# Optimization experiments

Hardware: AMD Instinct MI355X
Metric: run time of the kernel (lower is better)

The kernel has to match this reference:

```python
import jax, jax.numpy as jnp
import numpy as np

N, DIM, T = 131072, 1024, 256  # tokens, signature dim, num_tiles


def setup_inputs() -> dict:
    key = jax.random.key(0)
    k1, k2, k3 = jax.random.split(key, 3)
    x = jax.random.normal(k1, (N, DIM), dtype=jnp.float32)
    base = jax.random.uniform(k2, (DIM,), dtype=jnp.float32, minval=-1.0, maxval=1.0)
    deltas = jax.random.uniform(k3, (T - 1, DIM), dtype=jnp.float32, minval=-0.5, maxval=0.5)
    return {"x": x, "base": base, "deltas": deltas}


def _all_signatures(base, deltas):
    # base signature = sign(base); tile i>0: sig = sign(base*(1-|d|) + d*|d|), d = sign(delta_i)
    b = jnp.sign(base)                       # [DIM]
    d = jnp.sign(deltas)                     # [T-1, DIM]
    ad = jnp.abs(d)                          # |d| in {0,1}
    rest = jnp.sign(b[None, :] * (1.0 - ad) + d * ad)  # [T-1, DIM]
    return jnp.concatenate([b[None, :], rest], axis=0)  # [T, DIM]


def _hamming_distances(x, sigs):
    # 2-bit encoding: bit0 = (v>0), bit1 = (v<0).
    # Hamming dist over bits = sum(a) + sum(b) - 2*dot(a,b) per bit-plane (a^b = a+b-2ab for bits).
    px = (x > 0).astype(jnp.float32)          # [N, DIM]
    nx = (x < 0).astype(jnp.float32)
    ps = (sigs > 0).astype(jnp.float32)       # [T, DIM]
    ns = (sigs < 0).astype(jnp.float32)
    cross = px @ ps.T + nx @ ns.T             # [N, T] (single fused GEMM pair, K=DIM)
    pop_x = (px + nx).sum(axis=-1, keepdims=True)   # [N, 1]
    pop_s = (ps + ns).sum(axis=-1)[None, :]         # [1, T]
    return pop_x + pop_s - 2.0 * cross        # [N, T]


def reference(x, base, deltas):
    sigs = _all_signatures(base, deltas)       # [T, DIM] ternary
    distances = _hamming_distances(x, sigs)    # [N, T] (integer-valued float32)
    tile_idx = jnp.argmin(distances, axis=-1)  # [N]
    return tile_idx, distances
```

## Files before the change

kernel.cpp:

```cpp
#include <hip/hip_runtime.h>

typedef unsigned int u32;

#define NTOK 131072
#define DIMS 1024
#define NT   256

using bf16x8 = __attribute__((ext_vector_type(8))) short;
using f32x4  = __attribute__((ext_vector_type(4))) float;

#define BF_OFF   0
#define SV_OFF   (1 << 20)
#define FLAG_OFF ((1 << 20) + 1024)

__device__ __forceinline__ short sgnbf(float v) {
    return v > 0.f ? (short)0x3F80 : (v < 0.f ? (short)0xBF80 : (short)0);
}
__device__ __forceinline__ short absbf(float v) {
    return v != 0.f ? (short)0x3F80 : (short)0;
}

__global__ void sig_kernel(const float* __restrict__ base,
                           const float* __restrict__ deltas,
                           short* __restrict__ Bf,
                           float* __restrict__ Sv,
                           int* __restrict__ flags)
{
    const int t  = blockIdx.x;
    const int l  = threadIdx.x;
    const int ks = l >> 1;
    int nz = 0, zany = 0;
    #pragma unroll
    for (int gh = 0; gh < 2; ++gh) {
        const int g = (l & 1) * 2 + gh;
        bf16x8 a8, u8;
        #pragma unroll
        for (int j = 0; j < 8; ++j) {
            const int d  = ks * 32 + g * 8 + j;
            const float b  = base[d];
            const float dl = (t > 0) ? deltas[(size_t)(t - 1) * DIMS + d] : 0.f;
            const float s  = (dl != 0.f) ? dl : b;
            a8[j] = sgnbf(s);
            u8[j] = absbf(s);
            nz   += (s != 0.f) ? 1 : 0;
            zany |= (s == 0.f) ? 1 : 0;
        }
        const int L    = g * 16 + (t & 15);
        const int n    = t >> 4;
        const int slot = n ^ (t & 15);
        const size_t off = (size_t)L * 128 + slot * 8;
        *(bf16x8*)(Bf + (((size_t)0 * 32 + ks) << 13) + off) = a8;
        *(bf16x8*)(Bf + (((size_t)1 * 32 + ks) << 13) + off) = u8;
    }
    #pragma unroll
    for (int off = 1; off < 64; off <<= 1) nz += __shfl_xor(nz, off);
    const bool za = __any(zany != 0);
    if (l == 0) { Sv[t] = (float)nz; flags[t] = za ? 1 : 0; }
}

__global__ __launch_bounds__(256, 2)
void dist_kernel(const float* __restrict__ x,
                 const short* __restrict__ Bf,
                 const float* __restrict__ Sv,
                 const int* __restrict__ flags,
                 float* __restrict__ idx_out,
                 float* __restrict__ dist_out)
{
    __shared__ short lds[2][16384];

    const int lane = threadIdx.x & 63;
    const int w    = threadIdx.x >> 6;
    const int tok0 = blockIdx.x * 128 + w * 32;
    const int mrow = lane & 15;
    const int g    = lane >> 4;

    const int ff = flags[lane] | flags[64 + lane] | flags[128 + lane] | flags[192 + lane];
    const bool sigz = __any(ff != 0);

    const float* __restrict__ xr0 = x + (size_t)(tok0 + mrow) * DIMS + g * 8;
    const float* __restrict__ xr1 = x + (size_t)(tok0 + 16 + mrow) * DIMS + g * 8;

    f32x4 acc0[16], acc1[16];
    #pragma unroll
    for (int n = 0; n < 16; ++n) {
        acc0[n] = (f32x4){0.f, 0.f, 0.f, 0.f};
        acc1[n] = (f32x4){0.f, 0.f, 0.f, 0.f};
    }

    auto STAGE = [&](int b, int p, int kb) {
        #pragma unroll
        for (int s = 0; s < 2; ++s) {
            const short* src = Bf + (((size_t)p * 32 + 2 * kb + s) << 13) + w * 2048 + lane * 8;
            #pragma unroll
            for (int i = 0; i < 4; ++i) {
                __builtin_amdgcn_global_load_lds(
                    (const __attribute__((address_space(1))) u32*)(src + i * 512),
                    (__attribute__((address_space(3))) u32*)(&lds[b][s * 8192 + w * 2048 + i * 512]),
                    16, 0, 0);
            }
        }
    };

    int nz0 = 0, nz1 = 0;
    const int nplanes = sigz ? 2 : 1;

    for (int p = 0; p < nplanes; ++p) {
        STAGE(0, p, 0);
        float4 xv[8];
        xv[0] = *(const float4*)(xr0);       xv[1] = *(const float4*)(xr0 + 4);
        xv[2] = *(const float4*)(xr0 + 32);  xv[3] = *(const float4*)(xr0 + 36);
        xv[4] = *(const float4*)(xr1);       xv[5] = *(const float4*)(xr1 + 4);
        xv[6] = *(const float4*)(xr1 + 32);  xv[7] = *(const float4*)(xr1 + 36);

        for (int kb = 0; kb < 16; ++kb) {
            __syncthreads();

            float4 nx[8];
            if (kb < 15) {
                STAGE((kb + 1) & 1, p, kb + 1);
                const int o = (kb + 1) * 64;
                nx[0] = *(const float4*)(xr0 + o);      nx[1] = *(const float4*)(xr0 + o + 4);
                nx[2] = *(const float4*)(xr0 + o + 32); nx[3] = *(const float4*)(xr0 + o + 36);
                nx[4] = *(const float4*)(xr1 + o);      nx[5] = *(const float4*)(xr1 + o + 4);
                nx[6] = *(const float4*)(xr1 + o + 32); nx[7] = *(const float4*)(xr1 + o + 36);
            }

            if (p == 1) {
                #pragma unroll
                for (int i = 0; i < 4; ++i) {
                    nz0 += (xv[i][0]!=0.f)+(xv[i][1]!=0.f)+(xv[i][2]!=0.f)+(xv[i][3]!=0.f);
                    nz1 += (xv[4+i][0]!=0.f)+(xv[4+i][1]!=0.f)+(xv[4+i][2]!=0.f)+(xv[4+i][3]!=0.f);
                }
            }

            #pragma unroll
            for (int s = 0; s < 2; ++s) {
                const float4 a0 = xv[2 * s], a1 = xv[2 * s + 1];
                const float4 b0 = xv[4 + 2 * s], b1 = xv[4 + 2 * s + 1];
                bf16x8 f0, f1;
                if (p == 0) {
                    f0[0]=sgnbf(a0.x); f0[1]=sgnbf(a0.y); f0[2]=sgnbf(a0.z); f0[3]=sgnbf(a0.w);
                    f0[4]=sgnbf(a1.x); f0[5]=sgnbf(a1.y); f0[6]=sgnbf(a1.z); f0[7]=sgnbf(a1.w);
                    f1[0]=sgnbf(b0.x); f1[1]=sgnbf(b0.y); f1[2]=sgnbf(b0.z); f1[3]=sgnbf(b0.w);
                    f1[4]=sgnbf(b1.x); f1[5]=sgnbf(b1.y); f1[6]=sgnbf(b1.z); f1[7]=sgnbf(b1.w);
                } else {
                    f0[0]=absbf(a0.x); f0[1]=absbf(a0.y); f0[2]=absbf(a0.z); f0[3]=absbf(a0.w);
                    f0[4]=absbf(a1.x); f0[5]=absbf(a1.y); f0[6]=absbf(a1.z); f0[7]=absbf(a1.w);
                    f1[0]=absbf(b0.x); f1[1]=absbf(b0.y); f1[2]=absbf(b0.z); f1[3]=absbf(b0.w);
                    f1[4]=absbf(b1.x); f1[5]=absbf(b1.y); f1[6]=absbf(b1.z); f1[7]=absbf(b1.w);
                }

                const short* sa = &lds[kb & 1][s * 8192];
                __builtin_amdgcn_s_setprio(1);
                #pragma unroll
                for (int n = 0; n < 16; ++n) {
                    const bf16x8 ba = *(const bf16x8*)(sa + lane * 128 + ((n ^ mrow) & 15) * 8);
                    acc0[n] = __builtin_amdgcn_mfma_f32_16x16x32_bf16(f0, ba, acc0[n], 0, 0, 0);
                    acc1[n] = __builtin_amdgcn_mfma_f32_16x16x32_bf16(f1, ba, acc1[n], 0, 0, 0);
                }
                __builtin_amdgcn_s_setprio(0);
            }

            #pragma unroll
            for (int i = 0; i < 8; ++i) xv[i] = nx[i];
        }
        __syncthreads();
    }

    float su0r[4], su1r[4];
    if (sigz) {
        nz0 += __shfl_xor(nz0, 16); nz0 += __shfl_xor(nz0, 32);
        nz1 += __shfl_xor(nz1, 16); nz1 += __shfl_xor(nz1, 32);
        const float s0 = (float)nz0, s1 = (float)nz1;
        #pragma unroll
        for (int r = 0; r < 4; ++r) {
            su0r[r] = __shfl(s0, g * 4 + r);
            su1r[r] = __shfl(s1, g * 4 + r);
        }
    }

    int key0[4] = {0x7fffffff,0x7fffffff,0x7fffffff,0x7fffffff};
    int key1[4] = {0x7fffffff,0x7fffffff,0x7fffffff,0x7fffffff};
    #pragma unroll
    for (int n = 0; n < 16; ++n) {
        const int tile = n * 16 + mrow;
        const float svv = sigz ? Sv[tile] : 0.f;
        #pragma unroll
        for (int r = 0; r < 4; ++r) {
            const float dv0 = sigz ? (su0r[r] + svv - acc0[n][r]) : (1024.f - acc0[n][r]);
            const float dv1 = sigz ? (su1r[r] + svv - acc1[n][r]) : (1024.f - acc1[n][r]);
            dist_out[(size_t)(tok0 + g * 4 + r) * NT + tile]      = dv0;
            dist_out[(size_t)(tok0 + 16 + g * 4 + r) * NT + tile] = dv1;
            key0[r] = min(key0[r], ((int)dv0 << 8) | tile);
            key1[r] = min(key1[r], ((int)dv1 << 8) | tile);
        }
    }
    #pragma unroll
    for (int off = 1; off < 16; off <<= 1) {
        #pragma unroll
        for (int r = 0; r < 4; ++r) {
            key0[r] = min(key0[r], __shfl_xor(key0[r], off));
            key1[r] = min(key1[r], __shfl_xor(key1[r], off));
        }
    }
    if (mrow == 0) {
        #pragma unroll
        for (int r = 0; r < 4; ++r) {
            idx_out[tok0 + g * 4 + r]      = (float)(key0[r] & 255);
            idx_out[tok0 + 16 + g * 4 + r] = (float)(key1[r] & 255);
        }
    }
}

extern "C" void kernel_launch(void* const* d_in, const int* in_sizes, int n_in,
                              void* d_out, int out_size, void* d_ws, size_t ws_size,
                              hipStream_t stream)
{
    const float* x      = (const float*)d_in[0];
    const float* base   = (const float*)d_in[1];
    const float* deltas = (const float*)d_in[2];

    short* Bf  = (short*)((char*)d_ws + BF_OFF);
    float* Sv  = (float*)((char*)d_ws + SV_OFF);
    int* flags = (int*)((char*)d_ws + FLAG_OFF);

    float* idx_out  = (float*)d_out;
    float* dist_out = idx_out + NTOK;

    sig_kernel<<<NT, 64, 0, stream>>>(base, deltas, Bf, Sv, flags);
    dist_kernel<<<NTOK / 128, 256, 0, stream>>>(x, Bf, Sv, flags, idx_out, dist_out);
}
```

Measured before the change: 189.1 us.

## Deepen x prefetch to two stages with explicit vmcnt waits in the no-zero path

For the common case where signatures have no zeros, the main loop now keeps three register buffers of x, loading two k-blocks ahead. It replaces __syncthreads with an explicit partial s_waitcnt vmcnt plus s_barrier, and uses sched_barrier to pin the order of LDS staging, conversion and MFMA issue. The goal is to hide global-load latency for x and the LDS fill behind the MFMA work. The cost is more live registers, and the hand-counted vmcnt value is fragile if the compiler changes how many loads it emits. The zero-containing path keeps the old two-plane loop but drops setprio.

```diff
diff --git a/kernel.cpp b/kernel.cpp
--- a/kernel.cpp
+++ b/kernel.cpp
@@ -101,70 +101,123 @@
         }
     };
 
+    auto XLOAD = [&](float4* dst, int kb) {
+        const int o = kb * 64;
+        dst[0] = *(const float4*)(xr0 + o);      dst[1] = *(const float4*)(xr0 + o + 4);
+        dst[2] = *(const float4*)(xr0 + o + 32); dst[3] = *(const float4*)(xr0 + o + 36);
+        dst[4] = *(const float4*)(xr1 + o);      dst[5] = *(const float4*)(xr1 + o + 4);
+        dst[6] = *(const float4*)(xr1 + o + 32); dst[7] = *(const float4*)(xr1 + o + 36);
+    };
+
     int nz0 = 0, nz1 = 0;
-    const int nplanes = sigz ? 2 : 1;
-
-    for (int p = 0; p < nplanes; ++p) {
-        STAGE(0, p, 0);
-        float4 xv[8];
-        xv[0] = *(const float4*)(xr0);       xv[1] = *(const float4*)(xr0 + 4);
-        xv[2] = *(const float4*)(xr0 + 32);  xv[3] = *(const float4*)(xr0 + 36);
-        xv[4] = *(const float4*)(xr1);       xv[5] = *(const float4*)(xr1 + 4);
-        xv[6] = *(const float4*)(xr1 + 32);  xv[7] = *(const float4*)(xr1 + 36);
+
+    if (!sigz) {
+        float4 xv0[8], xv1[8], xv2[8];
+        #pragma unroll
+        for (int i = 0; i < 8; ++i) xv2[i] = (float4){0.f, 0.f, 0.f, 0.f};
+
+        STAGE(0, 0, 0);
+        __builtin_amdgcn_sched_barrier(0);
+        XLOAD(xv0, 0);
+        __builtin_amdgcn_sched_barrier(0);
+        XLOAD(xv1, 1);
+        __builtin_amdgcn_sched_barrier(0);
 
         for (int kb = 0; kb < 16; ++kb) {
+            if (kb < 15) asm volatile("s_waitcnt vmcnt(8)" ::: "memory");
+            else         asm volatile("s_waitcnt vmcnt(0)" ::: "memory");
+            __builtin_amdgcn_s_barrier();
+            __builtin_amdgcn_sched_barrier(0);
+
+            if (kb < 15) STAGE((kb + 1) & 1, 0, kb + 1);
+            __builtin_amdgcn_sched_barrier(0);
+
+            bf16x8 fA0, fA1, fB0, fB1;
+            #pragma unroll
+            for (int j = 0; j < 4; ++j) {
+                fA0[j]     = sgnbf(xv0[0][j]); fA0[4 + j] = sgnbf(xv0[1][j]);
+                fB0[j]     = sgnbf(xv0[2][j]); fB0[4 + j] = sgnbf(xv0[3][j]);
+                fA1[j]     = sgnbf(xv0[4][j]); fA1[4 + j] = sgnbf(xv0[5][j]);
+                fB1[j]     = sgnbf(xv0[6][j]); fB1[4 + j] = sgnbf(xv0[7][j]);
+            }
+
+            if (kb < 14) XLOAD(xv2, kb + 2);
+            __builtin_amdgcn_sched_barrier(0);
+
+            const short* sa0 = &lds[kb & 1][0];
+            const short* sa1 = &lds[kb & 1][8192];
+            __builtin_amdgcn_s_setprio(1);
+            #pragma unroll
+            for (int n = 0; n < 16; ++n) {
+                const bf16x8 ba = *(const bf16x8*)(sa0 + lane * 128 + ((n ^ mrow) & 15) * 8);
+                acc0[n] = __builtin_amdgcn_mfma_f32_16x16x32_bf16(fA0, ba, acc0[n], 0, 0, 0);
+                acc1[n] = __builtin_amdgcn_mfma_f32_16x16x32_bf16(fA1, ba, acc1[n], 0, 0, 0);
+            }
+            #pragma unroll
+            for (int n = 0; n < 16; ++n) {
+                const bf16x8 ba = *(const bf16x8*)(sa1 + lane * 128 + ((n ^ mrow) & 15) * 8);
+                acc0[n] = __builtin_amdgcn_mfma_f32_16x16x32_bf16(fB0, ba, acc0[n], 0, 0, 0);
+                acc1[n] = __builtin_amdgcn_mfma_f32_16x16x32_bf16(fB1, ba, acc1[n], 0, 0, 0);
+            }
+            __builtin_amdgcn_s_setprio(0);
+
+            #pragma unroll
+            for (int i = 0; i < 8; ++i) { xv0[i] = xv1[i]; xv1[i] = xv2[i]; }
+        }
+    } else {
+        for (int p = 0; p < 2; ++p) {
+            STAGE(0, p, 0);
+            float4 xv[8];
+            XLOAD(xv, 0);
+
+            for (int kb = 0; kb < 16; ++kb) {
+                __syncthreads();
+
+                float4 nx[8];
+                if (kb < 15) {
+                    STAGE((kb + 1) & 1, p, kb + 1);
+                    XLOAD(nx, kb + 1);
+                }
+
+                if (p == 1) {
+                    #pragma unroll
+                    for (int i = 0; i < 4; ++i) {
+                        nz0 += (xv[i][0]!=0.f)+(xv[i][1]!=0.f)+(xv[i][2]!=0.f)+(xv[i][3]!=0.f);
+                        nz1 += (xv[4+i][0]!=0.f)+(xv[4+i][1]!=0.f)+(xv[4+i][2]!=0.f)+(xv[4+i][3]!=0.f);
+                    }
+                }
+
+                #pragma unroll
+                for (int s = 0; s < 2; ++s) {
+                    const float4 a0 = xv[2 * s], a1 = xv[2 * s + 1];
+                    const float4 b0 = xv[4 + 2 * s], b1 = xv[4 + 2 * s + 1];
+                    bf16x8 f0, f1;
+                    if (p == 0) {
+                        f0[0]=sgnbf(a0.x); f0[1]=sgnbf(a0.y); f0[2]=sgnbf(a0.z); f0[3]=sgnbf(a0.w);
+                        f0[4]=sgnbf(a1.x); f0[5]=sgnbf(a1.y); f0[6]=sgnbf(a1.z); f0[7]=sgnbf(a1.w);
+                        f1[0]=sgnbf(b0.x); f1[1]=sgnbf(b0.y); f1[2]=sgnbf(b0.z); f1[3]=sgnbf(b0.w);
+                        f1[4]=sgnbf(b1.x); f1[5]=sgnbf(b1.y); f1[6]=sgnbf(b1.z); f1[7]=sgnbf(b1.w);
+                    } else {
+                        f0[0]=absbf(a0.x); f0[1]=absbf(a0.y); f0[2]=absbf(a0.z); f0[3]=absbf(a0.w);
+                        f0[4]=absbf(a1.x); f0[5]=absbf(a1.y); f0[6]=absbf(a1.z); f0[7]=absbf(a1.w);
+                        f1[0]=absbf(b0.x); f1[1]=absbf(b0.y); f1[2]=absbf(b0.z); f1[3]=absbf(b0.w);
+                        f1[4]=absbf(b1.x); f1[5]=absbf(b1.y); f1[6]=absbf(b1.z); f1[7]=absbf(b1.w);
+                    }
+
+                    const short* sa = &lds[kb & 1][s * 8192];
+                    #pragma unroll
+                    for (int n = 0; n < 16; ++n) {
+                        const bf16x8 ba = *(const bf16x8*)(sa + lane * 128 + ((n ^ mrow) & 15) * 8);
+                        acc0[n] = __builtin_amdgcn_mfma_f32_16x16x32_bf16(f0, ba, acc0[n], 0, 0, 0);
+                        acc1[n] = __builtin_amdgcn_mfma_f32_16x16x32_bf16(f1, ba, acc1[n], 0, 0, 0);
+                    }
+                }
+
+                #pragma unroll
+                for (int i = 0; i < 8; ++i) xv[i] = nx[i];
+            }
             __syncthreads();
-
-            float4 nx[8];
-            if (kb < 15) {
-                STAGE((kb + 1) & 1, p, kb + 1);
-                const int o = (kb + 1) * 64;
-                nx[0] = *(const float4*)(xr0 + o);      nx[1] = *(const float4*)(xr0 + o + 4);
-                nx[2] = *(const float4*)(xr0 + o + 32); nx[3] = *(const float4*)(xr0 + o + 36);
-                nx[4] = *(const float4*)(xr1 + o);      nx[5] = *(const float4*)(xr1 + o + 4);
-                nx[6] = *(const float4*)(xr1 + o + 32); nx[7] = *(const float4*)(xr1 + o + 36);
-            }
-
-            if (p == 1) {
-                #pragma unroll
-                for (int i = 0; i < 4; ++i) {
-                    nz0 += (xv[i][0]!=0.f)+(xv[i][1]!=0.f)+(xv[i][2]!=0.f)+(xv[i][3]!=0.f);
-                    nz1 += (xv[4+i][0]!=0.f)+(xv[4+i][1]!=0.f)+(xv[4+i][2]!=0.f)+(xv[4+i][3]!=0.f);
-                }
-            }
-
-            #pragma unroll
-            for (int s = 0; s < 2; ++s) {
-                const float4 a0 = xv[2 * s], a1 = xv[2 * s + 1];
-                const float4 b0 = xv[4 + 2 * s], b1 = xv[4 + 2 * s + 1];
-                bf16x8 f0, f1;
-                if (p == 0) {
-                    f0[0]=sgnbf(a0.x); f0[1]=sgnbf(a0.y); f0[2]=sgnbf(a0.z); f0[3]=sgnbf(a0.w);
-                    f0[4]=sgnbf(a1.x); f0[5]=sgnbf(a1.y); f0[6]=sgnbf(a1.z); f0[7]=sgnbf(a1.w);
-                    f1[0]=sgnbf(b0.x); f1[1]=sgnbf(b0.y); f1[2]=sgnbf(b0.z); f1[3]=sgnbf(b0.w);
-                    f1[4]=sgnbf(b1.x); f1[5]=sgnbf(b1.y); f1[6]=sgnbf(b1.z); f1[7]=sgnbf(b1.w);
-                } else {
-                    f0[0]=absbf(a0.x); f0[1]=absbf(a0.y); f0[2]=absbf(a0.z); f0[3]=absbf(a0.w);
-                    f0[4]=absbf(a1.x); f0[5]=absbf(a1.y); f0[6]=absbf(a1.z); f0[7]=absbf(a1.w);
-                    f1[0]=absbf(b0.x); f1[1]=absbf(b0.y); f1[2]=absbf(b0.z); f1[3]=absbf(b0.w);
-                    f1[4]=absbf(b1.x); f1[5]=absbf(b1.y); f1[6]=absbf(b1.z); f1[7]=absbf(b1.w);
-                }
-
-                const short* sa = &lds[kb & 1][s * 8192];
-                __builtin_amdgcn_s_setprio(1);
-                #pragma unroll
-                for (int n = 0; n < 16; ++n) {
-                    const bf16x8 ba = *(const bf16x8*)(sa + lane * 128 + ((n ^ mrow) & 15) * 8);
-                    acc0[n] = __builtin_amdgcn_mfma_f32_16x16x32_bf16(f0, ba, acc0[n], 0, 0, 0);
-                    acc1[n] = __builtin_amdgcn_mfma_f32_16x16x32_bf16(f1, ba, acc1[n], 0, 0, 0);
-                }
-                __builtin_amdgcn_s_setprio(0);
-            }
-
-            #pragma unroll
-            for (int i = 0; i < 8; ++i) xv[i] = nx[i];
-        }
-        __syncthreads();
+        }
     }
 
     float su0r[4], su1r[4];
```

Result: slower. 195.9 us (+3.6%).

## Warp-specialize dist kernel with producer waves converting x into LDS

Applied to the files above, without the earlier changes.

Adds two producer waves per block that load x with a three-deep register prefetch, convert it to bf16 sign values and write it into a double-buffered LDS tile. The four consumer waves only DMA the signature panel and run MFMAs, synchronized with raw barriers. The k-step is halved to 32 elements, so there are more barrier rounds. The aim is to take x loading and conversion off the MFMA critical path. The block grows to 384 threads, which may lower occupancy, and the synchronization is hand-tuned and fragile.

```diff
diff --git a/kernel.cpp b/kernel.cpp
--- a/kernel.cpp
+++ b/kernel.cpp
@@ -1,6 +1,7 @@
 #include <hip/hip_runtime.h>
 
 typedef unsigned int u32;
+typedef unsigned short u16;
 
 #define NTOK 131072
 #define DIMS 1024
@@ -58,7 +59,7 @@
     if (l == 0) { Sv[t] = (float)nz; flags[t] = za ? 1 : 0; }
 }
 
-__global__ __launch_bounds__(256, 2)
+__global__ __launch_bounds__(384)
 void dist_kernel(const float* __restrict__ x,
                  const short* __restrict__ Bf,
                  const float* __restrict__ Sv,
@@ -66,19 +67,19 @@
                  float* __restrict__ idx_out,
                  float* __restrict__ dist_out)
 {
-    __shared__ short lds[2][16384];
+    __shared__ short lds_b[2][8192];
+    __shared__ short lds_a[2][4096];
 
     const int lane = threadIdx.x & 63;
     const int w    = threadIdx.x >> 6;
-    const int tok0 = blockIdx.x * 128 + w * 32;
+    const int bid  = blockIdx.x;
     const int mrow = lane & 15;
     const int g    = lane >> 4;
 
     const int ff = flags[lane] | flags[64 + lane] | flags[128 + lane] | flags[192 + lane];
     const bool sigz = __any(ff != 0);
 
-    const float* __restrict__ xr0 = x + (size_t)(tok0 + mrow) * DIMS + g * 8;
-    const float* __restrict__ xr1 = x + (size_t)(tok0 + 16 + mrow) * DIMS + g * 8;
+    const int tok0 = bid * 128 + (w < 4 ? w * 32 : 0);
 
     f32x4 acc0[16], acc1[16];
     #pragma unroll
@@ -86,128 +87,182 @@
         acc0[n] = (f32x4){0.f, 0.f, 0.f, 0.f};
         acc1[n] = (f32x4){0.f, 0.f, 0.f, 0.f};
     }
-
-    auto STAGE = [&](int b, int p, int kb) {
-        #pragma unroll
-        for (int s = 0; s < 2; ++s) {
-            const short* src = Bf + (((size_t)p * 32 + 2 * kb + s) << 13) + w * 2048 + lane * 8;
-            #pragma unroll
-            for (int i = 0; i < 4; ++i) {
-                __builtin_amdgcn_global_load_lds(
-                    (const __attribute__((address_space(1))) u32*)(src + i * 512),
-                    (__attribute__((address_space(3))) u32*)(&lds[b][s * 8192 + w * 2048 + i * 512]),
-                    16, 0, 0);
-            }
+    int nz0 = 0, nz1 = 0;
+
+    auto BDMA = [&](int buf, int p, int ks) {
+        const short* src = Bf + (((size_t)p * 32 + ks) << 13) + w * 2048 + lane * 8;
+        #pragma unroll
+        for (int i = 0; i < 4; ++i) {
+            __builtin_amdgcn_global_load_lds(
+                (const __attribute__((address_space(1))) u32*)(src + i * 512),
+                (__attribute__((address_space(3))) u32*)(&lds_b[buf][w * 2048 + i * 512]),
+                16, 0, 0);
         }
     };
 
-    int nz0 = 0, nz1 = 0;
-    const int nplanes = sigz ? 2 : 1;
-
-    for (int p = 0; p < nplanes; ++p) {
-        STAGE(0, p, 0);
-        float4 xv[8];
-        xv[0] = *(const float4*)(xr0);       xv[1] = *(const float4*)(xr0 + 4);
-        xv[2] = *(const float4*)(xr0 + 32);  xv[3] = *(const float4*)(xr0 + 36);
-        xv[4] = *(const float4*)(xr1);       xv[5] = *(const float4*)(xr1 + 4);
-        xv[6] = *(const float4*)(xr1 + 32);  xv[7] = *(const float4*)(xr1 + 36);
-
-        for (int kb = 0; kb < 16; ++kb) {
-            __syncthreads();
-
-            float4 nx[8];
-            if (kb < 15) {
-                STAGE((kb + 1) & 1, p, kb + 1);
-                const int o = (kb + 1) * 64;
-                nx[0] = *(const float4*)(xr0 + o);      nx[1] = *(const float4*)(xr0 + o + 4);
-                nx[2] = *(const float4*)(xr0 + o + 32); nx[3] = *(const float4*)(xr0 + o + 36);
-                nx[4] = *(const float4*)(xr1 + o);      nx[5] = *(const float4*)(xr1 + o + 4);
-                nx[6] = *(const float4*)(xr1 + o + 32); nx[7] = *(const float4*)(xr1 + o + 36);
-            }
-
-            if (p == 1) {
-                #pragma unroll
-                for (int i = 0; i < 4; ++i) {
-                    nz0 += (xv[i][0]!=0.f)+(xv[i][1]!=0.f)+(xv[i][2]!=0.f)+(xv[i][3]!=0.f);
-                    nz1 += (xv[4+i][0]!=0.f)+(xv[4+i][1]!=0.f)+(xv[4+i][2]!=0.f)+(xv[4+i][3]!=0.f);
-                }
-            }
-
-            #pragma unroll
-            for (int s = 0; s < 2; ++s) {
-                const float4 a0 = xv[2 * s], a1 = xv[2 * s + 1];
-                const float4 b0 = xv[4 + 2 * s], b1 = xv[4 + 2 * s + 1];
-                bf16x8 f0, f1;
-                if (p == 0) {
-                    f0[0]=sgnbf(a0.x); f0[1]=sgnbf(a0.y); f0[2]=sgnbf(a0.z); f0[3]=sgnbf(a0.w);
-                    f0[4]=sgnbf(a1.x); f0[5]=sgnbf(a1.y); f0[6]=sgnbf(a1.z); f0[7]=sgnbf(a1.w);
-                    f1[0]=sgnbf(b0.x); f1[1]=sgnbf(b0.y); f1[2]=sgnbf(b0.z); f1[3]=sgnbf(b0.w);
-                    f1[4]=sgnbf(b1.x); f1[5]=sgnbf(b1.y); f1[6]=sgnbf(b1.z); f1[7]=sgnbf(b1.w);
-                } else {
-                    f0[0]=absbf(a0.x); f0[1]=absbf(a0.y); f0[2]=absbf(a0.z); f0[3]=absbf(a0.w);
-                    f0[4]=absbf(a1.x); f0[5]=absbf(a1.y); f0[6]=absbf(a1.z); f0[7]=absbf(a1.w);
-                    f1[0]=absbf(b0.x); f1[1]=absbf(b0.y); f1[2]=absbf(b0.z); f1[3]=absbf(b0.w);
-                    f1[4]=absbf(b1.x); f1[5]=absbf(b1.y); f1[6]=absbf(b1.z); f1[7]=absbf(b1.w);
-                }
-
-                const short* sa = &lds[kb & 1][s * 8192];
+    if (!sigz) {
+        if (w < 4) {
+            BDMA(0, 0, 0);
+            asm volatile("s_waitcnt vmcnt(0)" ::: "memory");
+            __builtin_amdgcn_s_barrier();
+            __builtin_amdgcn_sched_barrier(0);
+
+            for (int kb = 0; kb < 32; ++kb) {
+                if (kb < 31) BDMA((kb + 1) & 1, 0, kb + 1);
+
+                const short* sa = &lds_a[kb & 1][0];
+                const short* sb = &lds_b[kb & 1][0];
+                const bf16x8 a0 = *(const bf16x8*)(sa + (w * 32 + mrow) * 32 + g * 8);
+                const bf16x8 a1 = *(const bf16x8*)(sa + (w * 32 + 16 + mrow) * 32 + g * 8);
+
                 __builtin_amdgcn_s_setprio(1);
                 #pragma unroll
                 for (int n = 0; n < 16; ++n) {
-                    const bf16x8 ba = *(const bf16x8*)(sa + lane * 128 + ((n ^ mrow) & 15) * 8);
-                    acc0[n] = __builtin_amdgcn_mfma_f32_16x16x32_bf16(f0, ba, acc0[n], 0, 0, 0);
-                    acc1[n] = __builtin_amdgcn_mfma_f32_16x16x32_bf16(f1, ba, acc1[n], 0, 0, 0);
+                    const bf16x8 b = *(const bf16x8*)(sb + lane * 128 + ((n ^ mrow) & 15) * 8);
+                    acc0[n] = __builtin_amdgcn_mfma_f32_16x16x32_bf16(a0, b, acc0[n], 0, 0, 0);
+                    acc1[n] = __builtin_amdgcn_mfma_f32_16x16x32_bf16(a1, b, acc1[n], 0, 0, 0);
                 }
                 __builtin_amdgcn_s_setprio(0);
-            }
-
-            #pragma unroll
-            for (int i = 0; i < 8; ++i) xv[i] = nx[i];
-        }
-        __syncthreads();
-    }
-
-    float su0r[4], su1r[4];
-    if (sigz) {
-        nz0 += __shfl_xor(nz0, 16); nz0 += __shfl_xor(nz0, 32);
-        nz1 += __shfl_xor(nz1, 16); nz1 += __shfl_xor(nz1, 32);
-        const float s0 = (float)nz0, s1 = (float)nz1;
-        #pragma unroll
-        for (int r = 0; r < 4; ++r) {
-            su0r[r] = __shfl(s0, g * 4 + r);
-            su1r[r] = __shfl(s1, g * 4 + r);
-        }
-    }
-
-    int key0[4] = {0x7fffffff,0x7fffffff,0x7fffffff,0x7fffffff};
-    int key1[4] = {0x7fffffff,0x7fffffff,0x7fffffff,0x7fffffff};
-    #pragma unroll
-    for (int n = 0; n < 16; ++n) {
-        const int tile = n * 16 + mrow;
-        const float svv = sigz ? Sv[tile] : 0.f;
-        #pragma unroll
-        for (int r = 0; r < 4; ++r) {
-            const float dv0 = sigz ? (su0r[r] + svv - acc0[n][r]) : (1024.f - acc0[n][r]);
-            const float dv1 = sigz ? (su1r[r] + svv - acc1[n][r]) : (1024.f - acc1[n][r]);
-            dist_out[(size_t)(tok0 + g * 4 + r) * NT + tile]      = dv0;
-            dist_out[(size_t)(tok0 + 16 + g * 4 + r) * NT + tile] = dv1;
-            key0[r] = min(key0[r], ((int)dv0 << 8) | tile);
-            key1[r] = min(key1[r], ((int)dv1 << 8) | tile);
-        }
-    }
-    #pragma unroll
-    for (int off = 1; off < 16; off <<= 1) {
-        #pragma unroll
-        for (int r = 0; r < 4; ++r) {
-            key0[r] = min(key0[r], __shfl_xor(key0[r], off));
-            key1[r] = min(key1[r], __shfl_xor(key1[r], off));
-        }
-    }
-    if (mrow == 0) {
-        #pragma unroll
-        for (int r = 0; r < 4; ++r) {
-            idx_out[tok0 + g * 4 + r]      = (float)(key0[r] & 255);
-            idx_out[tok0 + 16 + g * 4 + r] = (float)(key1[r] & 255);
+
+                if (kb < 31) {
+                    asm volatile("s_waitcnt vmcnt(0)" ::: "memory");
+                    __builtin_amdgcn_s_barrier();
+                    __builtin_amdgcn_sched_barrier(0);
+                }
+            }
+        } else {
+            const int j = w - 4;
+            const float* xp = x + ((size_t)(bid * 128 + j * 64 + (lane >> 3))) * DIMS
+                            + (lane & 7) * 4;
+
+            float4 xb0[8], xb1[8], xb2[8];
+
+            auto XISSUE = [&](float4* dst, int m) {
+                #pragma unroll
+                for (int i = 0; i < 8; ++i)
+                    dst[i] = *(const float4*)(xp + (size_t)i * 8 * DIMS + m * 32);
+            };
+            auto CONVWRITE = [&](const float4* src, int buf) {
+                #pragma unroll
+                for (int i = 0; i < 8; ++i) {
+                    const u32 lo = (u32)(u16)sgnbf(src[i].x) | ((u32)(u16)sgnbf(src[i].y) << 16);
+                    const u32 hi = (u32)(u16)sgnbf(src[i].z) | ((u32)(u16)sgnbf(src[i].w) << 16);
+                    uint2 v; v.x = lo; v.y = hi;
+                    *(uint2*)&lds_a[buf][(j * 64 + i * 8 + (lane >> 3)) * 32 + (lane & 7) * 4] = v;
+                }
+            };
+
+            XISSUE(xb0, 0);
+            CONVWRITE(xb0, 0);
+            XISSUE(xb1, 1);
+            XISSUE(xb2, 2);
+            asm volatile("s_waitcnt lgkmcnt(0)" ::: "memory");
+            __builtin_amdgcn_s_barrier();
+            __builtin_amdgcn_sched_barrier(0);
+
+            #define PPHASE(KB, CUR, TGT) {                                   \
+                CONVWRITE(CUR, ((KB) + 1) & 1);                              \
+                if ((KB) <= 28) XISSUE(TGT, (KB) + 3);                       \
+                asm volatile("s_waitcnt lgkmcnt(0)" ::: "memory");           \
+                __builtin_amdgcn_s_barrier();                                \
+                __builtin_amdgcn_sched_barrier(0);                           \
+            }
+            for (int kbb = 0; kbb < 30; kbb += 3) {
+                PPHASE(kbb + 0, xb1, xb0)
+                PPHASE(kbb + 1, xb2, xb1)
+                PPHASE(kbb + 2, xb0, xb2)
+            }
+            PPHASE(30, xb1, xb0)
+            #undef PPHASE
+        }
+    } else {
+        const float* xr0 = x + (size_t)(tok0 + mrow) * DIMS + g * 8;
+        const float* xr1 = x + (size_t)(tok0 + 16 + mrow) * DIMS + g * 8;
+
+        for (int p = 0; p < 2; ++p) {
+            if (w < 4) BDMA(0, p, 0);
+            __syncthreads();
+            for (int kb = 0; kb < 32; ++kb) {
+                if (w < 4) {
+                    if (kb < 31) BDMA((kb + 1) & 1, p, kb + 1);
+
+                    const float4 v00 = *(const float4*)(xr0 + kb * 32);
+                    const float4 v01 = *(const float4*)(xr0 + kb * 32 + 4);
+                    const float4 v10 = *(const float4*)(xr1 + kb * 32);
+                    const float4 v11 = *(const float4*)(xr1 + kb * 32 + 4);
+
+                    bf16x8 f0, f1;
+                    #pragma unroll
+                    for (int jj = 0; jj < 4; ++jj) {
+                        f0[jj]     = p ? absbf(v00[jj]) : sgnbf(v00[jj]);
+                        f0[4 + jj] = p ? absbf(v01[jj]) : sgnbf(v01[jj]);
+                        f1[jj]     = p ? absbf(v10[jj]) : sgnbf(v10[jj]);
+                        f1[4 + jj] = p ? absbf(v11[jj]) : sgnbf(v11[jj]);
+                    }
+                    if (p == 1) {
+                        #pragma unroll
+                        for (int jj = 0; jj < 4; ++jj) {
+                            nz0 += (v00[jj] != 0.f) + (v01[jj] != 0.f);
+                            nz1 += (v10[jj] != 0.f) + (v11[jj] != 0.f);
+                        }
+                    }
+
+                    const short* sb = &lds_b[kb & 1][0];
+                    #pragma unroll
+                    for (int n = 0; n < 16; ++n) {
+                        const bf16x8 b = *(const bf16x8*)(sb + lane * 128 + ((n ^ mrow) & 15) * 8);
+                        acc0[n] = __builtin_amdgcn_mfma_f32_16x16x32_bf16(f0, b, acc0[n], 0, 0, 0);
+                        acc1[n] = __builtin_amdgcn_mfma_f32_16x16x32_bf16(f1, b, acc1[n], 0, 0, 0);
+                    }
+                }
+                __syncthreads();
+            }
+        }
+    }
+
+    if (w < 4) {
+        float su0r[4], su1r[4];
+        if (sigz) {
+            nz0 += __shfl_xor(nz0, 16); nz0 += __shfl_xor(nz0, 32);
+            nz1 += __shfl_xor(nz1, 16); nz1 += __shfl_xor(nz1, 32);
+            const float s0 = (float)nz0, s1 = (float)nz1;
+            #pragma unroll
+            for (int r = 0; r < 4; ++r) {
+                su0r[r] = __shfl(s0, g * 4 + r);
+                su1r[r] = __shfl(s1, g * 4 + r);
+            }
+        }
+
+        int key0[4] = {0x7fffffff,0x7fffffff,0x7fffffff,0x7fffffff};
+        int key1[4] = {0x7fffffff,0x7fffffff,0x7fffffff,0x7fffffff};
+        #pragma unroll
+        for (int n = 0; n < 16; ++n) {
+            const int tile = n * 16 + mrow;
+            const float svv = sigz ? Sv[tile] : 0.f;
+            #pragma unroll
+            for (int r = 0; r < 4; ++r) {
+                const float dv0 = sigz ? (su0r[r] + svv - acc0[n][r]) : (1024.f - acc0[n][r]);
+                const float dv1 = sigz ? (su1r[r] + svv - acc1[n][r]) : (1024.f - acc1[n][r]);
+                dist_out[(size_t)(tok0 + g * 4 + r) * NT + tile]      = dv0;
+                dist_out[(size_t)(tok0 + 16 + g * 4 + r) * NT + tile] = dv1;
+                key0[r] = min(key0[r], ((int)dv0 << 8) | tile);
+                key1[r] = min(key1[r], ((int)dv1 << 8) | tile);
+            }
+        }
+        #pragma unroll
+        for (int off = 1; off < 16; off <<= 1) {
+            #pragma unroll
+            for (int r = 0; r < 4; ++r) {
+                key0[r] = min(key0[r], __shfl_xor(key0[r], off));
+                key1[r] = min(key1[r], __shfl_xor(key1[r], off));
+            }
+        }
+        if (mrow == 0) {
+            #pragma unroll
+            for (int r = 0; r < 4; ++r) {
+                idx_out[tok0 + g * 4 + r]      = (float)(key0[r] & 255);
+                idx_out[tok0 + 16 + g * 4 + r] = (float)(key1[r] & 255);
+            }
         }
     }
 }
@@ -228,5 +283,5 @@
     float* dist_out = idx_out + NTOK;
 
     sig_kernel<<<NT, 64, 0, stream>>>(base, deltas, Bf, Sv, flags);
-    dist_kernel<<<NTOK / 128, 256, 0, stream>>>(x, Bf, Sv, flags, idx_out, dist_out);
-}
+    dist_kernel<<<NTOK / 128, 384, 0, stream>>>(x, Bf, Sv, flags, idx_out, dist_out);
+}
```

Result: slower. 203.6 us (+7.7%).

## Switch ternary GEMM to fp8 MFMA with padded LDS layout and quarter-K staging

Applied to the files above, without the earlier changes.

Encodes the ternary sign/abs values as fp8 (0x38 = 1.0) instead of bf16, and uses the 16x16x32 fp8 MFMA. This halves the signature bytes held in LDS and read from it. Staging changes from double-buffered global_load_lds copies of 16 K-blocks to four quarter-K loads through registers into a single 136-byte-padded LDS buffer, with two barriers per stage. The exact-integer results stay exact, but staging no longer overlaps compute, and the register-path copies add latency and VGPR pressure.

```diff
diff --git a/kernel.cpp b/kernel.cpp
--- a/kernel.cpp
+++ b/kernel.cpp
@@ -1,28 +1,41 @@
 #include <hip/hip_runtime.h>
 
 typedef unsigned int u32;
+typedef unsigned long long u64;
 
 #define NTOK 131072
 #define DIMS 1024
 #define NT   256
 
-using bf16x8 = __attribute__((ext_vector_type(8))) short;
-using f32x4  = __attribute__((ext_vector_type(4))) float;
+using f32x4 = __attribute__((ext_vector_type(4))) float;
 
 #define BF_OFF   0
+#define PL_STR   278528
+#define KQ_STR   69632
 #define SV_OFF   (1 << 20)
 #define FLAG_OFF ((1 << 20) + 1024)
 
-__device__ __forceinline__ short sgnbf(float v) {
-    return v > 0.f ? (short)0x3F80 : (v < 0.f ? (short)0xBF80 : (short)0);
-}
-__device__ __forceinline__ short absbf(float v) {
-    return v != 0.f ? (short)0x3F80 : (short)0;
+__device__ __forceinline__ u32 sgn8(float v) {
+    return v > 0.f ? 0x38u : (v < 0.f ? 0xB8u : 0u);
+}
+__device__ __forceinline__ u32 abs8(float v) {
+    return v != 0.f ? 0x38u : 0u;
+}
+__device__ __forceinline__ u64 pack8(float4 a, float4 b, int p) {
+    u32 lo, hi;
+    if (p == 0) {
+        lo = sgn8(a.x) | (sgn8(a.y) << 8) | (sgn8(a.z) << 16) | (sgn8(a.w) << 24);
+        hi = sgn8(b.x) | (sgn8(b.y) << 8) | (sgn8(b.z) << 16) | (sgn8(b.w) << 24);
+    } else {
+        lo = abs8(a.x) | (abs8(a.y) << 8) | (abs8(a.z) << 16) | (abs8(a.w) << 24);
+        hi = abs8(b.x) | (abs8(b.y) << 8) | (abs8(b.z) << 16) | (abs8(b.w) << 24);
+    }
+    return (u64)lo | ((u64)hi << 32);
 }
 
 __global__ void sig_kernel(const float* __restrict__ base,
                            const float* __restrict__ deltas,
-                           short* __restrict__ Bf,
+                           char* __restrict__ Bf8,
                            float* __restrict__ Sv,
                            int* __restrict__ flags)
 {
@@ -33,24 +46,30 @@
     #pragma unroll
     for (int gh = 0; gh < 2; ++gh) {
         const int g = (l & 1) * 2 + gh;
-        bf16x8 a8, u8;
+        float sv[8];
         #pragma unroll
         for (int j = 0; j < 8; ++j) {
             const int d  = ks * 32 + g * 8 + j;
             const float b  = base[d];
             const float dl = (t > 0) ? deltas[(size_t)(t - 1) * DIMS + d] : 0.f;
             const float s  = (dl != 0.f) ? dl : b;
-            a8[j] = sgnbf(s);
-            u8[j] = absbf(s);
+            sv[j] = s;
             nz   += (s != 0.f) ? 1 : 0;
             zany |= (s == 0.f) ? 1 : 0;
         }
+        float4 v0, v1;
+        v0.x = sv[0]; v0.y = sv[1]; v0.z = sv[2]; v0.w = sv[3];
+        v1.x = sv[4]; v1.y = sv[5]; v1.z = sv[6]; v1.w = sv[7];
+        const u64 pa = pack8(v0, v1, 0);
+        const u64 pu = pack8(v0, v1, 1);
+
         const int L    = g * 16 + (t & 15);
         const int n    = t >> 4;
-        const int slot = n ^ (t & 15);
-        const size_t off = (size_t)L * 128 + slot * 8;
-        *(bf16x8*)(Bf + (((size_t)0 * 32 + ks) << 13) + off) = a8;
-        *(bf16x8*)(Bf + (((size_t)1 * 32 + ks) << 13) + off) = u8;
+        const int slot = (n ^ (t & 15)) & 15;
+        const size_t off = (size_t)(ks >> 3) * KQ_STR
+                         + (size_t)((ks & 7) * 64 + L) * 136 + slot * 8;
+        *(u64*)(Bf8 + off)           = pa;
+        *(u64*)(Bf8 + PL_STR + off)  = pu;
     }
     #pragma unroll
     for (int off = 1; off < 64; off <<= 1) nz += __shfl_xor(nz, off);
@@ -60,13 +79,13 @@
 
 __global__ __launch_bounds__(256, 2)
 void dist_kernel(const float* __restrict__ x,
-                 const short* __restrict__ Bf,
+                 const char* __restrict__ Bf8,
                  const float* __restrict__ Sv,
                  const int* __restrict__ flags,
                  float* __restrict__ idx_out,
                  float* __restrict__ dist_out)
 {
-    __shared__ short lds[2][16384];
+    __shared__ u64 ldsb[KQ_STR / 8];
 
     const int lane = threadIdx.x & 63;
     const int w    = threadIdx.x >> 6;
@@ -87,17 +106,19 @@
         acc1[n] = (f32x4){0.f, 0.f, 0.f, 0.f};
     }
 
-    auto STAGE = [&](int b, int p, int kb) {
-        #pragma unroll
-        for (int s = 0; s < 2; ++s) {
-            const short* src = Bf + (((size_t)p * 32 + 2 * kb + s) << 13) + w * 2048 + lane * 8;
+    auto STAGE = [&](int p, int kq) {
+        const char* src = Bf8 + (size_t)p * PL_STR + (size_t)kq * KQ_STR
+                        + w * 17408 + lane * 16;
+        char* dst = (char*)ldsb + w * 17408 + lane * 16;
+        #pragma unroll
+        for (int i0 = 0; i0 < 17; i0 += 5) {
+            uint4 tmp[5];
             #pragma unroll
-            for (int i = 0; i < 4; ++i) {
-                __builtin_amdgcn_global_load_lds(
-                    (const __attribute__((address_space(1))) u32*)(src + i * 512),
-                    (__attribute__((address_space(3))) u32*)(&lds[b][s * 8192 + w * 2048 + i * 512]),
-                    16, 0, 0);
-            }
+            for (int i = 0; i < 5; ++i)
+                if (i0 + i < 17) tmp[i] = *(const uint4*)(src + (i0 + i) * 1024);
+            #pragma unroll
+            for (int i = 0; i < 5; ++i)
+                if (i0 + i < 17) *(uint4*)(dst + (i0 + i) * 1024) = tmp[i];
         }
     };
 
@@ -105,66 +126,48 @@
     const int nplanes = sigz ? 2 : 1;
 
     for (int p = 0; p < nplanes; ++p) {
-        STAGE(0, p, 0);
-        float4 xv[8];
-        xv[0] = *(const float4*)(xr0);       xv[1] = *(const float4*)(xr0 + 4);
-        xv[2] = *(const float4*)(xr0 + 32);  xv[3] = *(const float4*)(xr0 + 36);
-        xv[4] = *(const float4*)(xr1);       xv[5] = *(const float4*)(xr1 + 4);
-        xv[6] = *(const float4*)(xr1 + 32);  xv[7] = *(const float4*)(xr1 + 36);
-
-        for (int kb = 0; kb < 16; ++kb) {
+        for (int kq = 0; kq < 4; ++kq) {
             __syncthreads();
-
-            float4 nx[8];
-            if (kb < 15) {
-                STAGE((kb + 1) & 1, p, kb + 1);
-                const int o = (kb + 1) * 64;
-                nx[0] = *(const float4*)(xr0 + o);      nx[1] = *(const float4*)(xr0 + o + 4);
-                nx[2] = *(const float4*)(xr0 + o + 32); nx[3] = *(const float4*)(xr0 + o + 36);
-                nx[4] = *(const float4*)(xr1 + o);      nx[5] = *(const float4*)(xr1 + o + 4);
-                nx[6] = *(const float4*)(xr1 + o + 32); nx[7] = *(const float4*)(xr1 + o + 36);
-            }
-
-            if (p == 1) {
-                #pragma unroll
-                for (int i = 0; i < 4; ++i) {
-                    nz0 += (xv[i][0]!=0.f)+(xv[i][1]!=0.f)+(xv[i][2]!=0.f)+(xv[i][3]!=0.f);
-                    nz1 += (xv[4+i][0]!=0.f)+(xv[4+i][1]!=0.f)+(xv[4+i][2]!=0.f)+(xv[4+i][3]!=0.f);
+            STAGE(p, kq);
+            __syncthreads();
+
+            float4 c0 = *(const float4*)(xr0 + kq * 256);
+            float4 c1 = *(const float4*)(xr0 + kq * 256 + 4);
+            float4 c2 = *(const float4*)(xr1 + kq * 256);
+            float4 c3 = *(const float4*)(xr1 + kq * 256 + 4);
+
+            for (int ks = 0; ks < 8; ++ks) {
+                float4 n0, n1, n2, n3;
+                if (ks < 7) {
+                    const int o = kq * 256 + (ks + 1) * 32;
+                    n0 = *(const float4*)(xr0 + o); n1 = *(const float4*)(xr0 + o + 4);
+                    n2 = *(const float4*)(xr1 + o); n3 = *(const float4*)(xr1 + o + 4);
                 }
-            }
-
-            #pragma unroll
-            for (int s = 0; s < 2; ++s) {
-                const float4 a0 = xv[2 * s], a1 = xv[2 * s + 1];
-                const float4 b0 = xv[4 + 2 * s], b1 = xv[4 + 2 * s + 1];
-                bf16x8 f0, f1;
-                if (p == 0) {
-                    f0[0]=sgnbf(a0.x); f0[1]=sgnbf(a0.y); f0[2]=sgnbf(a0.z); f0[3]=sgnbf(a0.w);
-                    f0[4]=sgnbf(a1.x); f0[5]=sgnbf(a1.y); f0[6]=sgnbf(a1.z); f0[7]=sgnbf(a1.w);
-                    f1[0]=sgnbf(b0.x); f1[1]=sgnbf(b0.y); f1[2]=sgnbf(b0.z); f1[3]=sgnbf(b0.w);
-                    f1[4]=sgnbf(b1.x); f1[5]=sgnbf(b1.y); f1[6]=sgnbf(b1.z); f1[7]=sgnbf(b1.w);
-                } else {
-                    f0[0]=absbf(a0.x); f0[1]=absbf(a0.y); f0[2]=absbf(a0.z); f0[3]=absbf(a0.w);
-                    f0[4]=absbf(a1.x); f0[5]=absbf(a1.y); f0[6]=absbf(a1.z); f0[7]=absbf(a1.w);
-                    f1[0]=absbf(b0.x); f1[1]=absbf(b0.y); f1[2]=absbf(b0.z); f1[3]=absbf(b0.w);
-                    f1[4]=absbf(b1.x); f1[5]=absbf(b1.y); f1[6]=absbf(b1.z); f1[7]=absbf(b1.w);
+
+                const u64 a0 = pack8(c0, c1, p);
+                const u64 a1 = pack8(c2, c3, p);
+                if (p == 1) {
+                    nz0 += (c0.x!=0.f)+(c0.y!=0.f)+(c0.z!=0.f)+(c0.w!=0.f)
+                         + (c1.x!=0.f)+(c1.y!=0.f)+(c1.z!=0.f)+(c1.w!=0.f);
+                    nz1 += (c2.x!=0.f)+(c2.y!=0.f)+(c2.z!=0.f)+(c2.w!=0.f)
+                         + (c3.x!=0.f)+(c3.y!=0.f)+(c3.z!=0.f)+(c3.w!=0.f);
                 }
 
-                const short* sa = &lds[kb & 1][s * 8192];
+                const char* rowb = (const char*)ldsb + (size_t)(ks * 64 + lane) * 136;
                 __builtin_amdgcn_s_setprio(1);
                 #pragma unroll
                 for (int n = 0; n < 16; ++n) {
-                    const bf16x8 ba = *(const bf16x8*)(sa + lane * 128 + ((n ^ mrow) & 15) * 8);
-                    acc0[n] = __builtin_amdgcn_mfma_f32_16x16x32_bf16(f0, ba, acc0[n], 0, 0, 0);
-                    acc1[n] = __builtin_amdgcn_mfma_f32_16x16x32_bf16(f1, ba, acc1[n], 0, 0, 0);
+                    const u64 b = *(const u64*)(rowb + (((n ^ mrow) & 15) * 8));
+                    acc0[n] = __builtin_amdgcn_mfma_f32_16x16x32_fp8_fp8(
+                        (long)a0, (long)b, acc0[n], 0, 0, 0);
+                    acc1[n] = __builtin_amdgcn_mfma_f32_16x16x32_fp8_fp8(
+                        (long)a1, (long)b, acc1[n], 0, 0, 0);
                 }
                 __builtin_amdgcn_s_setprio(0);
+
+                c0 = n0; c1 = n1; c2 = n2; c3 = n3;
             }
-
-            #pragma unroll
-            for (int i = 0; i < 8; ++i) xv[i] = nx[i];
-        }
-        __syncthreads();
+        }
     }
 
     float su0r[4], su1r[4];
@@ -220,13 +223,13 @@
     const float* base   = (const float*)d_in[1];
     const float* deltas = (const float*)d_in[2];
 
-    short* Bf  = (short*)((char*)d_ws + BF_OFF);
-    float* Sv  = (float*)((char*)d_ws + SV_OFF);
-    int* flags = (int*)((char*)d_ws + FLAG_OFF);
+    char*  Bf8   = (char*)d_ws + BF_OFF;
+    float* Sv    = (float*)((char*)d_ws + SV_OFF);
+    int*   flags = (int*)((char*)d_ws + FLAG_OFF);
 
     float* idx_out  = (float*)d_out;
     float* dist_out = idx_out + NTOK;
 
-    sig_kernel<<<NT, 64, 0, stream>>>(base, deltas, Bf, Sv, flags);
-    dist_kernel<<<NTOK / 128, 256, 0, stream>>>(x, Bf, Sv, flags, idx_out, dist_out);
-}
+    sig_kernel<<<NT, 64, 0, stream>>>(base, deltas, Bf8, Sv, flags);
+    dist_kernel<<<NTOK / 128, 256, 0, stream>>>(x, Bf8, Sv, flags, idx_out, dist_out);
+}
```

Result: slower. 200.1 us (+5.8%).
